# Kernel tuning notes

Hardware: AMD Instinct MI355X
Metric: run time of the kernel (lower is better)

The kernel has to match this reference:

```python
import jax, jax.numpy as jnp
import numpy as np

NA, NB = 40000, 40000
D_IN, D_OUT, H, C = 256, 256, 8, 32  # C = D_OUT // H
E = 400000
N_MP = 3


def setup_inputs() -> dict:
    key = jax.random.key(0)
    ks = jax.random.split(key, 16)
    s = 1.0 / np.sqrt(D_IN)
    inp = {
        "x_A": jax.random.normal(ks[0], (NA, D_IN), jnp.float32),
        "x_B": jax.random.normal(ks[1], (NB, D_IN), jnp.float32),
        "edge_ab": jax.random.randint(ks[2], (2, E), 0, NB, jnp.int32),  # src in A, dst in B
        "edge_ba": jax.random.randint(ks[3], (2, E), 0, NA, jnp.int32),  # src in B, dst in A
        "edge_aa": jax.random.randint(ks[4], (2, E), 0, NA, jnp.int32),  # src in A, dst in A
        "W_A": jax.random.normal(ks[5], (D_IN, D_OUT), jnp.float32) * s,
        "b_A": jnp.zeros((D_OUT,), jnp.float32),
        "W_B": jax.random.normal(ks[6], (D_IN, D_OUT), jnp.float32) * s,
        "b_B": jnp.zeros((D_OUT,), jnp.float32),
        "attn_l": jax.random.normal(ks[7], (N_MP, H, C), jnp.float32) * 0.1,
        "attn_r": jax.random.normal(ks[8], (N_MP, H, C), jnp.float32) * 0.1,
        "rel_l_A": jax.random.normal(ks[9], (H, C), jnp.float32) * 0.1,
        "rel_r_A": jax.random.normal(ks[10], (H, C), jnp.float32) * 0.1,
        "rel_l_B": jax.random.normal(ks[11], (H, C), jnp.float32) * 0.1,
        "rel_r_B": jax.random.normal(ks[12], (H, C), jnp.float32) * 0.1,
    }
    return inp


def _leaky(x):
    return jax.nn.leaky_relu(x, negative_slope=0.2)


def _gat_relation(h_src, edge, a_l, a_r, n_dst):
    """GAT-style edge attention + segment softmax + scatter-add.
    h_src: [N_src,H,C], edge: [2,E], a_l: [N_src,H], a_r: [N_dst,H]."""
    src, dst = edge[0], edge[1]
    e = _leaky(a_l[src] + a_r[dst])                      # [E,H]
    m = jax.ops.segment_max(e, dst, num_segments=n_dst)  # [N_dst,H]
    ex = jnp.exp(e - m[dst])
    denom = jax.ops.segment_sum(ex, dst, num_segments=n_dst)
    alpha = ex / denom[dst]                              # softmax over in-neighbors
    msg = h_src[src] * alpha[:, :, None]                 # [E,H,C]
    return jax.ops.segment_sum(msg, dst, num_segments=n_dst)  # [N_dst,H,C]


def _beta_combine(h, rel_embs, rel_l, rel_r):
    """Relation-level attention (get_beta_weights) + weighted sum.
    h: [N,H,C], rel_embs: [N,H,R,C]."""
    bl = (h * rel_l).sum(-1)                                 # [N,H]
    br = (rel_embs * rel_r[None, :, None, :]).sum(-1)        # [N,H,R]
    beta = jax.nn.softmax(_leaky(bl[:, :, None] + br), axis=2)
    out = (rel_embs * beta[..., None]).sum(2)                # [N,H,C]
    return out.reshape(out.shape[0], H * C)


def reference(x_A, x_B, edge_ab, edge_ba, edge_aa, W_A, b_A, W_B, b_B,
              attn_l, attn_r, rel_l_A, rel_r_A, rel_l_B, rel_r_B):
    nA, nB = x_A.shape[0], x_B.shape[0]
    h_A = (x_A @ W_A + b_A).reshape(nA, H, C)
    h_B = (x_B @ W_B + b_B).reshape(nB, H, C)

    # per-metapath node attention scalars (get_alphas)
    # metapath 0: A->B, 1: B->A, 2: A->A
    al0 = (h_A * attn_l[0]).sum(-1); ar0 = (h_B * attn_r[0]).sum(-1)
    al1 = (h_B * attn_l[1]).sum(-1); ar1 = (h_A * attn_r[1]).sum(-1)
    al2 = (h_A * attn_l[2]).sum(-1); ar2 = (h_A * attn_r[2]).sum(-1)

    # aggregate per tail relation (agg_relation_neighbors); last slot = self
    rel_ba = _gat_relation(h_B, edge_ba, al1, ar1, nA)
    rel_aa = _gat_relation(h_A, edge_aa, al2, ar2, nA)
    emb_A = jnp.stack([rel_ba, rel_aa, h_A], axis=2)         # [NA,H,3,C]

    rel_ab = _gat_relation(h_A, edge_ab, al0, ar0, nB)
    emb_B = jnp.stack([rel_ab, h_B], axis=2)                 # [NB,H,2,C]

    out_A = jax.nn.relu(_beta_combine(h_A, emb_A, rel_l_A, rel_r_A))
    out_B = jax.nn.relu(_beta_combine(h_B, emb_B, rel_l_B, rel_r_B))
    return jnp.concatenate([out_A, out_B], axis=0)           # [NA+NB, D_OUT]
```

## Files before the change

kernel.cpp:

```cpp
#include <hip/hip_runtime.h>
#include <math.h>

#define NAn 40000
#define NBn 40000
#define DIN 256
#define DOUT 256
#define NH 8
#define NC 32
#define NE 400000
#define CAP 64

typedef __attribute__((ext_vector_type(8))) short short8;
typedef __attribute__((ext_vector_type(4))) float floatx4;

__device__ __forceinline__ float leaky(float x) { return x > 0.f ? x : 0.2f * x; }
__device__ __forceinline__ unsigned bf16_rne_bits(float x) {
  unsigned u = __float_as_uint(x);
  unsigned r = u + 0x7fffu + ((u >> 16) & 1u);
  return r & 0xffff0000u;
}
__device__ __forceinline__ void bf8(uint4 u, float* f) {
  f[0] = __uint_as_float(u.x << 16);
  f[1] = __uint_as_float(u.x & 0xffff0000u);
  f[2] = __uint_as_float(u.y << 16);
  f[3] = __uint_as_float(u.y & 0xffff0000u);
  f[4] = __uint_as_float(u.z << 16);
  f[5] = __uint_as_float(u.z & 0xffff0000u);
  f[6] = __uint_as_float(u.w << 16);
  f[7] = __uint_as_float(u.w & 0xffff0000u);
}

__global__ void wswz(const float* __restrict__ WA, const float* __restrict__ WB,
                     short8* __restrict__ hiA, short8* __restrict__ hiB,
                     int* __restrict__ cnts) {
  int t = blockIdx.x * blockDim.x + threadIdx.x;
  for (int i = t; i < 3 * NAn; i += 16384) cnts[i] = 0;
  const float* W;
  short8* hi;
  int tt = t;
  if (tt < 8192) {
    W = WA; hi = hiA;
  } else {
    tt -= 8192;
    if (tt >= 8192) return;
    W = WB; hi = hiB;
  }
  int kt = tt >> 10, nt = (tt >> 6) & 15, l = tt & 63;
  int n = nt * 16 + (l & 15);
  int kb = kt * 32 + (l >> 4) * 8;
  short8 h8;
#pragma unroll
  for (int j = 0; j < 8; ++j) {
    float w = W[(size_t)(kb + j) * DOUT + n];
    h8[j] = (short)(bf16_rne_bits(w) >> 16);
  }
  hi[tt] = h8;
}

__global__ __launch_bounds__(256) void gemm_mfma(
    const float* __restrict__ XA, const float* __restrict__ XB,
    const short8* __restrict__ WAhi, const short8* __restrict__ WBhi,
    const float* __restrict__ bA, const float* __restrict__ bB,
    const float* __restrict__ attn_l, const float* __restrict__ attn_r,
    unsigned* __restrict__ HAbf, unsigned* __restrict__ HBbf,
    float* __restrict__ al0, float* __restrict__ ar1,
    float* __restrict__ al2, float* __restrict__ ar2,
    float* __restrict__ ar0, float* __restrict__ al1) {
  __shared__ short8 bfrag[2][1024];
  int blk = blockIdx.x;
  const bool isA = blk < (NAn / 64);
  const float* X;
  const short8* Wh;
  const float* bias;
  unsigned* Hbf;
  if (isA) {
    X = XA; Wh = WAhi; bias = bA; Hbf = HAbf;
  } else {
    blk -= NAn / 64;
    X = XB; Wh = WBhi; bias = bB; Hbf = HBbf;
  }
  const int tid = threadIdx.x;
  const int lane = tid & 63, wave = tid >> 6;
  const int row0 = blk * 64 + wave * 16;
  const int col16 = lane & 15, quad = lane >> 4;

  floatx4 acc[16];
#pragma unroll
  for (int i = 0; i < 16; ++i) acc[i] = (floatx4){0.f, 0.f, 0.f, 0.f};

  const float4* xp = (const float4*)(X + (size_t)(row0 + col16) * DIN) + quad * 2;

  uint4 pre[4];
  const uint4* wsrc = (const uint4*)Wh;
#pragma unroll
  for (int c = 0; c < 4; ++c) pre[c] = wsrc[c * 256 + tid];
  {
    uint4* d = (uint4*)&bfrag[0][0];
#pragma unroll
    for (int c = 0; c < 4; ++c) d[c * 256 + tid] = pre[c];
  }
  __syncthreads();

  for (int kt = 0; kt < 8; ++kt) {
    if (kt < 7) {
      const uint4* s = wsrc + (size_t)(kt + 1) * 1024;
#pragma unroll
      for (int c = 0; c < 4; ++c) pre[c] = s[c * 256 + tid];
    }
    float4 x0 = xp[kt * 8];
    float4 x1 = xp[kt * 8 + 1];
    float xv[8] = {x0.x, x0.y, x0.z, x0.w, x1.x, x1.y, x1.z, x1.w};
    short8 ahi, alo;
#pragma unroll
    for (int j = 0; j < 8; ++j) {
      unsigned hb = bf16_rne_bits(xv[j]);
      ahi[j] = (short)(hb >> 16);
      float rem = xv[j] - __uint_as_float(hb);
      alo[j] = (short)(bf16_rne_bits(rem) >> 16);
    }
    const short8* bp = &bfrag[kt & 1][0];
#pragma unroll
    for (int nt = 0; nt < 16; ++nt) {
      short8 bv = bp[nt * 64 + lane];
      acc[nt] = __builtin_amdgcn_mfma_f32_16x16x32_bf16(ahi, bv, acc[nt], 0, 0, 0);
      acc[nt] = __builtin_amdgcn_mfma_f32_16x16x32_bf16(alo, bv, acc[nt], 0, 0, 0);
    }
    if (kt < 7) {
      uint4* d = (uint4*)&bfrag[(kt + 1) & 1][0];
#pragma unroll
      for (int c = 0; c < 4; ++c) d[c * 256 + tid] = pre[c];
    }
    __syncthreads();
  }
  unsigned* lds_u = (unsigned*)&bfrag[0][0];
#pragma unroll
  for (int nt = 0; nt < 16; ++nt) {
    float bcol = bias[nt * 16 + col16];
#pragma unroll
    for (int r = 0; r < 4; ++r) {
      int rl = wave * 16 + quad * 4 + r;
      float v = acc[nt][r] + bcol;
      float vp = __shfl_xor(v, 1);
      if ((lane & 1) == 0) {
        unsigned p = (bf16_rne_bits(v) >> 16) | bf16_rne_bits(vp);
        Hbf[(size_t)(blk * 64 + rl) * 128 + nt * 8 + (col16 >> 1)] = p;
        lds_u[rl * 128 + nt * 8 + (col16 >> 1)] = p;
      }
    }
  }
  __syncthreads();
#pragma unroll
  for (int t = 0; t < 2; ++t) {
    int task = tid + t * 256;
    int rl = task >> 3, head = task & 7;
    int node = blk * 64 + rl;
    int k = node * 8 + head;
    float f[32];
    const uint4* lp = (const uint4*)(lds_u + rl * 128 + head * 16);
#pragma unroll
    for (int q = 0; q < 4; ++q) bf8(lp[q], &f[q * 8]);
    if (isA) {
      const float* l0 = attn_l + 0 * DOUT + head * NC;
      const float* r1 = attn_r + 1 * DOUT + head * NC;
      const float* l2 = attn_l + 2 * DOUT + head * NC;
      const float* r2 = attn_r + 2 * DOUT + head * NC;
      float s0 = 0, s1 = 0, s2 = 0, s3 = 0;
#pragma unroll
      for (int c = 0; c < 32; ++c) {
        s0 += f[c] * l0[c];
        s1 += f[c] * r1[c];
        s2 += f[c] * l2[c];
        s3 += f[c] * r2[c];
      }
      al0[k] = s0; ar1[k] = s1; al2[k] = s2; ar2[k] = s3;
    } else {
      const float* r0 = attn_r + 0 * DOUT + head * NC;
      const float* l1 = attn_l + 1 * DOUT + head * NC;
      float s0 = 0, s1 = 0;
#pragma unroll
      for (int c = 0; c < 32; ++c) {
        s0 += f[c] * r0[c];
        s1 += f[c] * l1[c];
      }
      ar0[k] = s0; al1[k] = s1;
    }
  }
}

__global__ void build_csr3(const int* __restrict__ e_ba, const int* __restrict__ e_aa,
                           const int* __restrict__ e_ab, int* __restrict__ cnt_ba,
                           int* __restrict__ cnt_aa, int* __restrict__ cnt_ab,
                           int* __restrict__ sl_ba, int* __restrict__ sl_aa,
                           int* __restrict__ sl_ab) {
  int i = blockIdx.x * blockDim.x + threadIdx.x;
  if (i >= 3 * NE) return;
  const int* e;
  int* cnt;
  int* sl;
  int k = i;
  if (i < NE) {
    e = e_ba; cnt = cnt_ba; sl = sl_ba;
  } else if (i < 2 * NE) {
    e = e_aa; cnt = cnt_aa; sl = sl_aa; k = i - NE;
  } else {
    e = e_ab; cnt = cnt_ab; sl = sl_ab; k = i - 2 * NE;
  }
  int src = __builtin_nontemporal_load(&e[k]);
  int dst = __builtin_nontemporal_load(&e[NE + k]);
  int pos = atomicAdd(&cnt[dst], 1);
  if (pos < CAP) __builtin_nontemporal_store(src, &sl[(size_t)dst * CAP + pos]);
}

__device__ __forceinline__ void gat2(int dst, int wave, int lane, int h, int sub, int head,
                                     const int* __restrict__ cnt,
                                     const int* __restrict__ slots,
                                     const float* __restrict__ al,
                                     const float* __restrict__ ar,
                                     const uint4* __restrict__ hbf,
                                     int lds_slot[4][64], float lds_ex[4][512],
                                     float acc[8]) {
#pragma unroll
  for (int k = 0; k < 8; ++k) acc[k] = 0.f;
  int deg = cnt[dst];
  if (deg > CAP) deg = CAP;
  if (deg == 0) return;
  __threadfence_block();
  if (lane < deg) {
    int s = slots[(size_t)dst * CAP + lane];
    lds_slot[wave][lane] = s;
    float4 a0 = *(const float4*)(al + (size_t)s * 8);
    float4 a1 = *(const float4*)(al + (size_t)s * 8 + 4);
    float4 r0 = *(const float4*)(ar + (size_t)dst * 8);
    float4 r1 = *(const float4*)(ar + (size_t)dst * 8 + 4);
    float* exq = &lds_ex[wave][lane * 8];
    exq[0] = __expf(leaky(a0.x + r0.x));
    exq[1] = __expf(leaky(a0.y + r0.y));
    exq[2] = __expf(leaky(a0.z + r0.z));
    exq[3] = __expf(leaky(a0.w + r0.w));
    exq[4] = __expf(leaky(a1.x + r1.x));
    exq[5] = __expf(leaky(a1.y + r1.y));
    exq[6] = __expf(leaky(a1.z + r1.z));
    exq[7] = __expf(leaky(a1.w + r1.w));
  }
  __threadfence_block();
  float den = 0.f;
  int iters = (deg + 1) >> 1;
  for (int it = 0; it < iters; ++it) {
    int j = it * 2 + h;
    if (j < deg) {
      int sj = lds_slot[wave][j];
      float w = lds_ex[wave][j * 8 + head];
      uint4 u = hbf[(size_t)sj * 32 + sub];
      den += w;
      float f[8];
      bf8(u, f);
#pragma unroll
      for (int k = 0; k < 8; ++k) acc[k] += w * f[k];
    }
  }
#pragma unroll
  for (int k = 0; k < 8; ++k) acc[k] += __shfl_xor(acc[k], 32);
  den += __shfl_xor(den, 32);
  float inv = 1.f / den;
#pragma unroll
  for (int k = 0; k < 8; ++k) acc[k] *= inv;
}

__global__ __launch_bounds__(256) void agg_combine(
    const int* __restrict__ cnt_ba, const int* __restrict__ sl_ba,
    const float* __restrict__ al1, const float* __restrict__ ar1,
    const int* __restrict__ cnt_aa, const int* __restrict__ sl_aa,
    const float* __restrict__ al2, const float* __restrict__ ar2,
    const int* __restrict__ cnt_ab, const int* __restrict__ sl_ab,
    const float* __restrict__ al0, const float* __restrict__ ar0,
    const uint4* __restrict__ hAbf, const uint4* __restrict__ hBbf,
    const float* __restrict__ rlA, const float* __restrict__ rrA,
    const float* __restrict__ rlB, const float* __restrict__ rrB,
    float* __restrict__ outp) {
  __shared__ int lds_slot[4][64];
  __shared__ float lds_ex[4][512];
  int wave = threadIdx.x >> 6, lane = threadIdx.x & 63;
  int h = lane >> 5, sub = lane & 31, head = sub >> 2;
  bool isA = blockIdx.x < (NAn / 4);
  int dst = (isA ? blockIdx.x : blockIdx.x - NAn / 4) * 4 + wave;
  float m0[8], hv[8], o[8];
  if (isA) {
    float m1[8];
    gat2(dst, wave, lane, h, sub, head, cnt_ba, sl_ba, al1, ar1, hBbf, lds_slot, lds_ex, m0);
    gat2(dst, wave, lane, h, sub, head, cnt_aa, sl_aa, al2, ar2, hAbf, lds_slot, lds_ex, m1);
    uint4 us = hAbf[(size_t)dst * 32 + sub];
    bf8(us, hv);
    const float4* rl4 = (const float4*)rlA;
    const float4* rr4 = (const float4*)rrA;
    float4 rl0 = rl4[sub * 2], rl1 = rl4[sub * 2 + 1];
    float4 rr0 = rr4[sub * 2], rr1 = rr4[sub * 2 + 1];
    float rl8[8] = {rl0.x, rl0.y, rl0.z, rl0.w, rl1.x, rl1.y, rl1.z, rl1.w};
    float rr8[8] = {rr0.x, rr0.y, rr0.z, rr0.w, rr1.x, rr1.y, rr1.z, rr1.w};
    float pbl = 0, p0 = 0, p1 = 0, p2 = 0;
#pragma unroll
    for (int k = 0; k < 8; ++k) {
      pbl += hv[k] * rl8[k];
      p0 += m0[k] * rr8[k];
      p1 += m1[k] * rr8[k];
      p2 += hv[k] * rr8[k];
    }
#pragma unroll
    for (int d = 1; d < 4; d <<= 1) {
      pbl += __shfl_xor(pbl, d);
      p0 += __shfl_xor(p0, d);
      p1 += __shfl_xor(p1, d);
      p2 += __shfl_xor(p2, d);
    }
    float b0 = leaky(pbl + p0), b1 = leaky(pbl + p1), b2 = leaky(pbl + p2);
    float mx = fmaxf(b0, fmaxf(b1, b2));
    float w0 = __expf(b0 - mx), w1 = __expf(b1 - mx), w2 = __expf(b2 - mx);
    float inv = 1.f / (w0 + w1 + w2);
    w0 *= inv; w1 *= inv; w2 *= inv;
#pragma unroll
    for (int k = 0; k < 8; ++k)
      o[k] = fmaxf(0.f, m0[k] * w0 + m1[k] * w1 + hv[k] * w2);
  } else {
    gat2(dst, wave, lane, h, sub, head, cnt_ab, sl_ab, al0, ar0, hAbf, lds_slot, lds_ex, m0);
    uint4 us = hBbf[(size_t)dst * 32 + sub];
    bf8(us, hv);
    const float4* rl4 = (const float4*)rlB;
    const float4* rr4 = (const float4*)rrB;
    float4 rl0 = rl4[sub * 2], rl1 = rl4[sub * 2 + 1];
    float4 rr0 = rr4[sub * 2], rr1 = rr4[sub * 2 + 1];
    float rl8[8] = {rl0.x, rl0.y, rl0.z, rl0.w, rl1.x, rl1.y, rl1.z, rl1.w};
    float rr8[8] = {rr0.x, rr0.y, rr0.z, rr0.w, rr1.x, rr1.y, rr1.z, rr1.w};
    float pbl = 0, p0 = 0, p1 = 0;
#pragma unroll
    for (int k = 0; k < 8; ++k) {
      pbl += hv[k] * rl8[k];
      p0 += m0[k] * rr8[k];
      p1 += hv[k] * rr8[k];
    }
#pragma unroll
    for (int d = 1; d < 4; d <<= 1) {
      pbl += __shfl_xor(pbl, d);
      p0 += __shfl_xor(p0, d);
      p1 += __shfl_xor(p1, d);
    }
    float b0 = leaky(pbl + p0), b1 = leaky(pbl + p1);
    float mx = fmaxf(b0, b1);
    float w0 = __expf(b0 - mx), w1 = __expf(b1 - mx);
    float inv = 1.f / (w0 + w1);
    w0 *= inv; w1 *= inv;
#pragma unroll
    for (int k = 0; k < 8; ++k) o[k] = fmaxf(0.f, m0[k] * w0 + hv[k] * w1);
  }
  float* orow = outp + (size_t)(isA ? dst : NAn + dst) * DOUT + sub * 8;
  if (h == 0) {
    *(float4*)orow = (float4){o[0], o[1], o[2], o[3]};
    *(float4*)(orow + 4) = (float4){o[4], o[5], o[6], o[7]};
  }
}

extern "C" void kernel_launch(void* const* d_in, const int* in_sizes, int n_in, void* d_out,
                              int out_size, void* d_ws, size_t ws_size, hipStream_t stream) {
  const float* xA = (const float*)d_in[0];
  const float* xB = (const float*)d_in[1];
  const int* e_ab = (const int*)d_in[2];
  const int* e_ba = (const int*)d_in[3];
  const int* e_aa = (const int*)d_in[4];
  const float* WA = (const float*)d_in[5];
  const float* bA = (const float*)d_in[6];
  const float* WB = (const float*)d_in[7];
  const float* bB = (const float*)d_in[8];
  const float* attn_l = (const float*)d_in[9];
  const float* attn_r = (const float*)d_in[10];
  const float* rlA = (const float*)d_in[11];
  const float* rrA = (const float*)d_in[12];
  const float* rlB = (const float*)d_in[13];
  const float* rrB = (const float*)d_in[14];
  float* out = (float*)d_out;

  char* p = (char*)d_ws;
  auto alloc = [&](size_t bytes) -> char* {
    char* r = p;
    p += (bytes + 255) & ~(size_t)255;
    return r;
  };
  unsigned* hAbf = (unsigned*)alloc((size_t)NAn * DOUT * 2);
  unsigned* hBbf = (unsigned*)alloc((size_t)NBn * DOUT * 2);
  float* al0 = (float*)alloc((size_t)NAn * NH * 4);
  float* ar1 = (float*)alloc((size_t)NAn * NH * 4);
  float* al2 = (float*)alloc((size_t)NAn * NH * 4);
  float* ar2 = (float*)alloc((size_t)NAn * NH * 4);
  float* ar0 = (float*)alloc((size_t)NBn * NH * 4);
  float* al1 = (float*)alloc((size_t)NBn * NH * 4);
  short8* WAhi = (short8*)alloc((size_t)8192 * 16);
  short8* WBhi = (short8*)alloc((size_t)8192 * 16);
  int* cnts = (int*)alloc((size_t)3 * NAn * 4);
  int* cnt_ba = cnts;
  int* cnt_aa = cnts + NAn;
  int* cnt_ab = cnts + 2 * NAn;
  int* slots_ba = (int*)alloc((size_t)NAn * CAP * 4);
  int* slots_aa = (int*)alloc((size_t)NAn * CAP * 4);
  int* slots_ab = (int*)alloc((size_t)NBn * CAP * 4);

  wswz<<<64, 256, 0, stream>>>(WA, WB, WAhi, WBhi, cnts);
  build_csr3<<<(3 * NE + 255) / 256, 256, 0, stream>>>(e_ba, e_aa, e_ab, cnt_ba, cnt_aa,
                                                       cnt_ab, slots_ba, slots_aa, slots_ab);
  gemm_mfma<<<(NAn + NBn) / 64, 256, 0, stream>>>(xA, xB, WAhi, WBhi, bA, bB, attn_l,
                                                  attn_r, hAbf, hBbf, al0, ar1, al2, ar2,
                                                  ar0, al1);
  agg_combine<<<(NAn + NBn) / 4, 256, 0, stream>>>(
      cnt_ba, slots_ba, al1, ar1, cnt_aa, slots_aa, al2, ar2, cnt_ab, slots_ab, al0, ar0,
      (const uint4*)hAbf, (const uint4*)hBbf, rlA, rrA, rlB, rrB, out);
}
```

Before: 474.6 us.

## Fuse CSR build into GEMM kernel and preload all A fragments

Merges the edge-bucketing kernel into the GEMM launch as extra leading blocks, so the atomic scatter work can overlap with the MFMA projection and one launch disappears. Inside the GEMM path, the block now loads all of its X rows up front and converts them to hi/lo bf16 fragments before the k-loop. The k-loop is fully unrolled, and launch bounds request 5 blocks per CU. The change also drops the nontemporal hints on the edge loads and stores. Holding all fragments in registers raises register pressure, which may conflict with the occupancy target or cause spills.

Result: no change. 475.3 us (+0.1%).

```diff
diff --git a/kernel.cpp b/kernel.cpp
--- a/kernel.cpp
+++ b/kernel.cpp
@@ -9,6 +9,8 @@
 #define NC 32
 #define NE 400000
 #define CAP 64
+#define GEMMB ((NAn + NBn) / 64)
+#define CSRB ((3 * NE + 255) / 256)
 
 typedef __attribute__((ext_vector_type(8))) short short8;
 typedef __attribute__((ext_vector_type(4))) float floatx4;
@@ -57,7 +59,7 @@
   hi[tt] = h8;
 }
 
-__global__ __launch_bounds__(256) void gemm_mfma(
+__global__ __launch_bounds__(256, 5) void gemm_csr(
     const float* __restrict__ XA, const float* __restrict__ XB,
     const short8* __restrict__ WAhi, const short8* __restrict__ WBhi,
     const float* __restrict__ bA, const float* __restrict__ bB,
@@ -65,9 +67,33 @@
     unsigned* __restrict__ HAbf, unsigned* __restrict__ HBbf,
     float* __restrict__ al0, float* __restrict__ ar1,
     float* __restrict__ al2, float* __restrict__ ar2,
-    float* __restrict__ ar0, float* __restrict__ al1) {
+    float* __restrict__ ar0, float* __restrict__ al1,
+    const int* __restrict__ e_ba, const int* __restrict__ e_aa,
+    const int* __restrict__ e_ab, int* __restrict__ cnt_ba,
+    int* __restrict__ cnt_aa, int* __restrict__ cnt_ab,
+    int* __restrict__ sl_ba, int* __restrict__ sl_aa, int* __restrict__ sl_ab) {
+  if (blockIdx.x < CSRB) {
+    int i = blockIdx.x * 256 + threadIdx.x;
+    if (i >= 3 * NE) return;
+    const int* e;
+    int* cnt;
+    int* sl;
+    int k = i;
+    if (i < NE) {
+      e = e_ba; cnt = cnt_ba; sl = sl_ba;
+    } else if (i < 2 * NE) {
+      e = e_aa; cnt = cnt_aa; sl = sl_aa; k = i - NE;
+    } else {
+      e = e_ab; cnt = cnt_ab; sl = sl_ab; k = i - 2 * NE;
+    }
+    int src = e[k];
+    int dst = e[NE + k];
+    int pos = atomicAdd(&cnt[dst], 1);
+    if (pos < CAP) sl[(size_t)dst * CAP + pos] = src;
+    return;
+  }
   __shared__ short8 bfrag[2][1024];
-  int blk = blockIdx.x;
+  int blk = blockIdx.x - CSRB;
   const bool isA = blk < (NAn / 64);
   const float* X;
   const short8* Wh;
@@ -81,49 +107,58 @@
   }
   const int tid = threadIdx.x;
   const int lane = tid & 63, wave = tid >> 6;
+  const int col16 = lane & 15, quad = lane >> 4;
   const int row0 = blk * 64 + wave * 16;
-  const int col16 = lane & 15, quad = lane >> 4;
-
-  floatx4 acc[16];
-#pragma unroll
-  for (int i = 0; i < 16; ++i) acc[i] = (floatx4){0.f, 0.f, 0.f, 0.f};
 
   const float4* xp = (const float4*)(X + (size_t)(row0 + col16) * DIN) + quad * 2;
+  const uint4* wsrc = (const uint4*)Wh;
 
   uint4 pre[4];
-  const uint4* wsrc = (const uint4*)Wh;
 #pragma unroll
   for (int c = 0; c < 4; ++c) pre[c] = wsrc[c * 256 + tid];
+
+  float4 xf[16];
+#pragma unroll
+  for (int j = 0; j < 16; ++j) xf[j] = xp[(j >> 1) * 8 + (j & 1)];
+
   {
     uint4* d = (uint4*)&bfrag[0][0];
 #pragma unroll
     for (int c = 0; c < 4; ++c) d[c * 256 + tid] = pre[c];
   }
+
+  short8 AH[8], AL[8];
+#pragma unroll
+  for (int kt = 0; kt < 8; ++kt) {
+    float xv[8] = {xf[2 * kt].x,     xf[2 * kt].y,     xf[2 * kt].z,     xf[2 * kt].w,
+                   xf[2 * kt + 1].x, xf[2 * kt + 1].y, xf[2 * kt + 1].z, xf[2 * kt + 1].w};
+#pragma unroll
+    for (int j = 0; j < 8; ++j) {
+      unsigned hb = bf16_rne_bits(xv[j]);
+      AH[kt][j] = (short)(hb >> 16);
+      float rem = xv[j] - __uint_as_float(hb);
+      AL[kt][j] = (short)(bf16_rne_bits(rem) >> 16);
+    }
+  }
+
+  floatx4 acc[16];
+#pragma unroll
+  for (int i = 0; i < 16; ++i) acc[i] = (floatx4){0.f, 0.f, 0.f, 0.f};
   __syncthreads();
 
+#pragma unroll
   for (int kt = 0; kt < 8; ++kt) {
     if (kt < 7) {
       const uint4* s = wsrc + (size_t)(kt + 1) * 1024;
 #pragma unroll
       for (int c = 0; c < 4; ++c) pre[c] = s[c * 256 + tid];
     }
-    float4 x0 = xp[kt * 8];
-    float4 x1 = xp[kt * 8 + 1];
-    float xv[8] = {x0.x, x0.y, x0.z, x0.w, x1.x, x1.y, x1.z, x1.w};
-    short8 ahi, alo;
-#pragma unroll
-    for (int j = 0; j < 8; ++j) {
-      unsigned hb = bf16_rne_bits(xv[j]);
-      ahi[j] = (short)(hb >> 16);
-      float rem = xv[j] - __uint_as_float(hb);
-      alo[j] = (short)(bf16_rne_bits(rem) >> 16);
-    }
     const short8* bp = &bfrag[kt & 1][0];
 #pragma unroll
     for (int nt = 0; nt < 16; ++nt) {
       short8 bv = bp[nt * 64 + lane];
-      acc[nt] = __builtin_amdgcn_mfma_f32_16x16x32_bf16(ahi, bv, acc[nt], 0, 0, 0);
-      acc[nt] = __builtin_amdgcn_mfma_f32_16x16x32_bf16(alo, bv, acc[nt], 0, 0, 0);
+      acc[nt] = __builtin_amdgcn_mfma_f32_16x16x32_bf16(AH[kt], bv, acc[nt], 0, 0, 0);
+      acc[nt] = __builtin_amdgcn_mfma_f32_16x16x32_bf16(AL[kt], bv, acc[nt], 0, 0, 0);
     }
     if (kt < 7) {
       uint4* d = (uint4*)&bfrag[(kt + 1) & 1][0];
@@ -185,30 +220,6 @@
       ar0[k] = s0; al1[k] = s1;
     }
   }
-}
-
-__global__ void build_csr3(const int* __restrict__ e_ba, const int* __restrict__ e_aa,
-                           const int* __restrict__ e_ab, int* __restrict__ cnt_ba,
-                           int* __restrict__ cnt_aa, int* __restrict__ cnt_ab,
-                           int* __restrict__ sl_ba, int* __restrict__ sl_aa,
-                           int* __restrict__ sl_ab) {
-  int i = blockIdx.x * blockDim.x + threadIdx.x;
-  if (i >= 3 * NE) return;
-  const int* e;
-  int* cnt;
-  int* sl;
-  int k = i;
-  if (i < NE) {
-    e = e_ba; cnt = cnt_ba; sl = sl_ba;
-  } else if (i < 2 * NE) {
-    e = e_aa; cnt = cnt_aa; sl = sl_aa; k = i - NE;
-  } else {
-    e = e_ab; cnt = cnt_ab; sl = sl_ab; k = i - 2 * NE;
-  }
-  int src = __builtin_nontemporal_load(&e[k]);
-  int dst = __builtin_nontemporal_load(&e[NE + k]);
-  int pos = atomicAdd(&cnt[dst], 1);
-  if (pos < CAP) __builtin_nontemporal_store(src, &sl[(size_t)dst * CAP + pos]);
 }
 
 __device__ __forceinline__ void gat2(int dst, int wave, int lane, int h, int sub, int head,
@@ -401,11 +412,9 @@
   int* slots_ab = (int*)alloc((size_t)NBn * CAP * 4);
 
   wswz<<<64, 256, 0, stream>>>(WA, WB, WAhi, WBhi, cnts);
-  build_csr3<<<(3 * NE + 255) / 256, 256, 0, stream>>>(e_ba, e_aa, e_ab, cnt_ba, cnt_aa,
-                                                       cnt_ab, slots_ba, slots_aa, slots_ab);
-  gemm_mfma<<<(NAn + NBn) / 64, 256, 0, stream>>>(xA, xB, WAhi, WBhi, bA, bB, attn_l,
-                                                  attn_r, hAbf, hBbf, al0, ar1, al2, ar2,
-                                                  ar0, al1);
+  gemm_csr<<<GEMMB + CSRB, 256, 0, stream>>>(
+      xA, xB, WAhi, WBhi, bA, bB, attn_l, attn_r, hAbf, hBbf, al0, ar1, al2, ar2, ar0, al1,
+      e_ba, e_aa, e_ab, cnt_ba, cnt_aa, cnt_ab, slots_ba, slots_aa, slots_ab);
   agg_combine<<<(NAn + NBn) / 4, 256, 0, stream>>>(
       cnt_ba, slots_ba, al1, ar1, cnt_aa, slots_aa, al2, ar2, cnt_ab, slots_ab, al0, ar0,
       (const uint4*)hAbf, (const uint4*)hBbf, rlA, rrA, rlB, rrB, out);
```
